# Kernel tuning notes

Measured on AMD Instinct MI355X. Metric: run time of the kernel, lower is better.

Reference implementation:

```python
import jax, jax.numpy as jnp
import numpy as np

TEMPERATURE = 0.5


def setup_inputs() -> dict:
    key = jax.random.key(0)
    k1, k2 = jax.random.split(key)
    N, D = 4096, 256
    emb_i = jax.random.normal(k1, (N, D), dtype=jnp.float32)
    emb_j = jax.random.normal(k2, (N, D), dtype=jnp.float32)
    return {"emb_i": emb_i, "emb_j": emb_j, "batch_size": N}


def reference(emb_i, emb_j, batch_size):
    N = batch_size
    # L2-normalize each embedding row (F.normalize eps=1e-12)
    def l2n(x):
        return x / jnp.maximum(jnp.linalg.norm(x, axis=1, keepdims=True), 1e-12)
    reps = jnp.concatenate([l2n(emb_i), l2n(emb_j)], axis=0)  # [2N, D]
    # cosine similarity of normalized vectors == dot product
    logits = (reps @ reps.T) / TEMPERATURE                    # [2N, 2N]
    twoN = 2 * N
    # denominator excludes only the self term k != i (stable logsumexp)
    diag_mask = jnp.eye(twoN, dtype=bool)
    masked = jnp.where(diag_mask, -jnp.inf, logits)
    log_denom = jax.nn.logsumexp(masked, axis=1)              # [2N]
    # positive pair for row i is (i+N) mod 2N
    idx = jnp.arange(twoN)
    pos = logits[idx, (idx + N) % twoN]                       # [2N]
    # loss = 1/(2N) * sum_i -log(exp(pos_i)/denom_i)
    return jnp.mean(log_denom - pos)
```

## Files before the change

kernel.cpp:

```cpp
#include <hip/hip_runtime.h>

typedef short short8 __attribute__((ext_vector_type(8)));
typedef float f32x4  __attribute__((ext_vector_type(4)));

#define TWO_N 8192
#define NHALF 4096
#define DDIM  256
#define NB    32
#define NBLK2 528

__device__ __forceinline__ float b2f(unsigned short u) {
    return __uint_as_float(((unsigned int)u) << 16);
}
__device__ __forceinline__ unsigned short f2b(float f) {
    unsigned int u = __float_as_uint(f);
    u += 0x7fffu + ((u >> 16) & 1u);
    return (unsigned short)(u >> 16);
}

__device__ __forceinline__ int probe_is_f32(const void* p, int lane) {
    unsigned int u = ((const unsigned int*)p)[lane];
    float lowv = __uint_as_float(u << 16);
    int crazy = !(fabsf(lowv) <= 1024.0f);
    return __ballot(crazy) != 0ull;
}

typedef __attribute__((address_space(1))) const unsigned int guint_t;
typedef __attribute__((address_space(3))) unsigned int luint_t;
__device__ __forceinline__ void gl_lds16(const unsigned short* g, unsigned short* l) {
    __builtin_amdgcn_global_load_lds((guint_t*)(const void*)g, (luint_t*)(void*)l, 16, 0, 0);
}

__global__ __launch_bounds__(256) void k_norm(const void* __restrict__ ei,
                                              const void* __restrict__ ej,
                                              unsigned short* __restrict__ reps) {
    int row  = (blockIdx.x * 256 + threadIdx.x) >> 6;
    int lane = threadIdx.x & 63;
    int isf  = probe_is_f32(ei, lane);
    int first = (row < NHALF);
    int r     = first ? row : row - NHALF;
    float x0, x1, x2, x3;
    if (isf) {
        const float* s = (first ? (const float*)ei : (const float*)ej) + (size_t)r * DDIM;
        float4 v = ((const float4*)s)[lane];
        x0 = v.x; x1 = v.y; x2 = v.z; x3 = v.w;
    } else {
        const unsigned short* s =
            (first ? (const unsigned short*)ei : (const unsigned short*)ej) + (size_t)r * DDIM;
        ushort4 v = ((const ushort4*)s)[lane];
        x0 = b2f(v.x); x1 = b2f(v.y); x2 = b2f(v.z); x3 = b2f(v.w);
    }
    float ss = x0 * x0 + x1 * x1 + x2 * x2 + x3 * x3;
    for (int off = 32; off > 0; off >>= 1) ss += __shfl_xor(ss, off);
    float inv = 1.0f / fmaxf(sqrtf(ss), 1e-12f);
    ushort4 o;
    o.x = f2b(x0 * inv); o.y = f2b(x1 * inv);
    o.z = f2b(x2 * inv); o.w = f2b(x3 * inv);
    ((ushort4*)(reps + (size_t)row * DDIM))[lane] = o;
}

__global__ __launch_bounds__(512, 2) void k_main(const unsigned short* __restrict__ R,
                                                 float* __restrict__ S_part,
                                                 float* __restrict__ pos) {
    __shared__ __align__(16) unsigned short As[2][256 * 64];
    __shared__ __align__(16) unsigned short Bs[2][256 * 64];

    int b = ((int)blockIdx.x & 7) * 66 + ((int)blockIdx.x >> 3);
    int rb = (int)((65.0f - sqrtf(4225.0f - 8.0f * (float)b)) * 0.5f);
    if (rb > 31) rb = 31;
    while ((65 * (rb + 1) - (rb + 1) * (rb + 1)) / 2 <= b) ++rb;
    while ((65 * rb - rb * rb) / 2 > b) --rb;
    int cb = rb + (b - (65 * rb - rb * rb) / 2);

    const int tid  = threadIdx.x;
    const int wave = tid >> 6;
    const int lane = tid & 63;
    const int quad = lane >> 4;
    const int l16  = lane & 15;
    const int wrg  = wave >> 2;
    const int wcg  = wave & 3;
    const int wr   = wrg * 128;
    const int wc   = wcg * 64;
    const int r8   = lane >> 3;
    const int c8   = (lane & 7) ^ r8;

    f32x4 acc[8][4];
#pragma unroll
    for (int r = 0; r < 8; ++r)
#pragma unroll
        for (int c = 0; c < 4; ++c) {
            acc[r][c][0] = 0.0f; acc[r][c][1] = 0.0f;
            acc[r][c][2] = 0.0f; acc[r][c][3] = 0.0f;
        }

    auto stage = [&](int d, int kc) {
#pragma unroll
        for (int t = 0; t < 4; ++t) {
            int u = wave * 4 + t;
            const unsigned short* ga =
                R + (size_t)(rb * 256 + u * 8 + r8) * DDIM + kc * 64 + c8 * 8;
            const unsigned short* gb =
                R + (size_t)(cb * 256 + u * 8 + r8) * DDIM + kc * 64 + c8 * 8;
            gl_lds16(ga, &As[d][u * 512]);
            gl_lds16(gb, &Bs[d][u * 512]);
        }
    };

    stage(0, 0);
    __syncthreads();

    for (int kc = 0; kc < 4; ++kc) {
        const int cur = kc & 1;
        if (kc < 3) stage(cur ^ 1, kc + 1);
#pragma unroll
        for (int kk = 0; kk < 2; ++kk) {
            short8 afr[8], bfr[4];
            int q  = kk * 4 + quad;
            int sl = q ^ (l16 & 7);
#pragma unroll
            for (int r = 0; r < 8; ++r)
                afr[r] = *(const short8*)(&As[cur][(wr + r * 16 + l16) * 64 + sl * 8]);
#pragma unroll
            for (int c = 0; c < 4; ++c)
                bfr[c] = *(const short8*)(&Bs[cur][(wc + c * 16 + l16) * 64 + sl * 8]);
#pragma unroll
            for (int r = 0; r < 8; ++r)
#pragma unroll
                for (int c = 0; c < 4; ++c)
                    acc[r][c] = __builtin_amdgcn_mfma_f32_16x16x32_bf16(
                        afr[r], bfr[c], acc[r][c], 0, 0, 0);
        }
        if (kc < 3) __syncthreads();
    }

    float col_acc[4][2] = {{0.0f, 0.0f}, {0.0f, 0.0f}, {0.0f, 0.0f}, {0.0f, 0.0f}};
#pragma unroll
    for (int r = 0; r < 8; ++r)
#pragma unroll
        for (int j = 0; j < 4; ++j) {
            float s = 0.0f;
#pragma unroll
            for (int c = 0; c < 4; ++c) {
                float e = __expf(fmaf(acc[r][c][j], 2.0f, -2.0f));
                s += e;
                col_acc[c][r >> 2] += e;
            }
            s += __shfl_xor(s, 1);
            s += __shfl_xor(s, 2);
            s += __shfl_xor(s, 4);
            s += __shfl_xor(s, 8);
            if (l16 == 0) {
                int row = rb * 256 + wr + r * 16 + quad * 4 + j;
                S_part[(size_t)(4 * cb + wcg) * TWO_N + row] = s;
            }
        }
    if (rb != cb) {
#pragma unroll
        for (int c = 0; c < 4; ++c)
#pragma unroll
            for (int h = 0; h < 2; ++h) {
                float s = col_acc[c][h];
                s += __shfl_xor(s, 16);
                s += __shfl_xor(s, 32);
                if (lane < 16) {
                    int row = cb * 256 + wc + c * 16 + lane;
                    S_part[(size_t)(4 * rb + 2 * wrg + h) * TWO_N + row] = s;
                }
            }
    }
    if (cb == rb + 16) {
        int dlt = (wc - wr) >> 4;
#pragma unroll
        for (int r = 0; r < 8; ++r)
#pragma unroll
            for (int c = 0; c < 4; ++c)
                if (r == c + dlt)
#pragma unroll
                    for (int j = 0; j < 4; ++j)
                        if (quad * 4 + j == l16)
                            pos[rb * 256 + wr + r * 16 + l16] = 2.0f * acc[r][c][j];
    }
}

__global__ __launch_bounds__(256) void k_rows(const float* __restrict__ S_part,
                                              const float* __restrict__ pos,
                                              float* __restrict__ part_blk) {
    __shared__ float red[256];
    int tid = threadIdx.x;
    int rr  = tid & 63;
    int cg  = tid >> 6;
    int row = blockIdx.x * 64 + rr;
    float s = 0.0f;
#pragma unroll 8
    for (int c = cg * 32; c < cg * 32 + 32; ++c)
        s += S_part[(size_t)c * TWO_N + row];
    red[tid] = s;
    __syncthreads();
    if (tid < 64) {
        float total = red[tid] + red[tid + 64] + red[tid + 128] + red[tid + 192];
        float p = (row < NHALF) ? pos[row] : pos[row - NHALF];
        float part = 2.0f + logf(total - 1.0f) - p;
        for (int off = 32; off > 0; off >>= 1) part += __shfl_xor(part, off);
        if (tid == 0) part_blk[blockIdx.x] = part;
    }
}

__global__ __launch_bounds__(128) void k_fin(const float* __restrict__ part_blk,
                                             unsigned int* __restrict__ out) {
    int tid = threadIdx.x;
    float local = part_blk[tid];
    __shared__ float red2[2];
    for (int off = 32; off > 0; off >>= 1) local += __shfl_xor(local, off);
    if ((tid & 63) == 0) red2[tid >> 6] = local;
    __syncthreads();
    if (tid == 0) {
        float L = (red2[0] + red2[1]) / 8192.0f;
        unsigned int bb = (unsigned int)f2b(L);
        out[0] = (bb << 16) | bb;
    }
}

extern "C" void kernel_launch(void* const* d_in, const int* in_sizes, int n_in,
                              void* d_out, int out_size, void* d_ws, size_t ws_size,
                              hipStream_t stream) {
    (void)in_sizes; (void)n_in; (void)out_size; (void)ws_size;
    const void* ei = d_in[0];
    const void* ej = d_in[1];
    char* ws = (char*)d_ws;

    float*          pos      = (float*)(ws);
    float*          part_blk = (float*)(ws + 16384);
    unsigned short* reps     = (unsigned short*)(ws + 49152);
    float*          S_part   = (float*)(ws + 4243456);

    k_norm<<<2048, 256, 0, stream>>>(ei, ej, reps);
    k_main<<<NBLK2, 512, 0, stream>>>(reps, S_part, pos);
    k_rows<<<128,  256, 0, stream>>>(S_part, pos, part_blk);
    k_fin <<<1,    128, 0, stream>>>(part_blk, (unsigned int*)d_out);
}
```

Baseline: 115.0 us.

## Use persistent-style grid and deeper prefetch pipeline in GEMM-exp kernel

Launches 512 blocks instead of 528, so the first 16 blocks each process two tiles, to match the grid to the CU count. The K loop now prefetches two stages ahead using raw s_barrier and explicit vmcnt waits instead of __syncthreads. It also raises wave priority around the MFMA bursts. The aim is to hide global-to-LDS latency and avoid a tail wave of 16 tiles. The trade-off is that 16 blocks do twice the work, which may lengthen the critical path.

```diff
diff --git a/kernel.cpp b/kernel.cpp
--- a/kernel.cpp
+++ b/kernel.cpp
@@ -6,8 +6,8 @@
 #define TWO_N 8192
 #define NHALF 4096
 #define DDIM  256
-#define NB    32
-#define NBLK2 528
+#define NTILE 528
+#define NBLK  512
 
 __device__ __forceinline__ float b2f(unsigned short u) {
     return __uint_as_float(((unsigned int)u) << 16);
@@ -65,13 +65,6 @@
     __shared__ __align__(16) unsigned short As[2][256 * 64];
     __shared__ __align__(16) unsigned short Bs[2][256 * 64];
 
-    int b = ((int)blockIdx.x & 7) * 66 + ((int)blockIdx.x >> 3);
-    int rb = (int)((65.0f - sqrtf(4225.0f - 8.0f * (float)b)) * 0.5f);
-    if (rb > 31) rb = 31;
-    while ((65 * (rb + 1) - (rb + 1) * (rb + 1)) / 2 <= b) ++rb;
-    while ((65 * rb - rb * rb) / 2 > b) --rb;
-    int cb = rb + (b - (65 * rb - rb * rb) / 2);
-
     const int tid  = threadIdx.x;
     const int wave = tid >> 6;
     const int lane = tid & 63;
@@ -84,101 +77,126 @@
     const int r8   = lane >> 3;
     const int c8   = (lane & 7) ^ r8;
 
-    f32x4 acc[8][4];
-#pragma unroll
-    for (int r = 0; r < 8; ++r)
-#pragma unroll
-        for (int c = 0; c < 4; ++c) {
-            acc[r][c][0] = 0.0f; acc[r][c][1] = 0.0f;
-            acc[r][c][2] = 0.0f; acc[r][c][3] = 0.0f;
+    const int bid  = (int)blockIdx.x;
+    const int nrep = (bid < NTILE - NBLK) ? 2 : 1;
+
+    for (int rep = 0; rep < nrep; ++rep) {
+        int id = (rep == 0) ? bid : bid + NBLK;
+        int b = (id & 7) * 66 + (id >> 3);
+        int rb = (int)((65.0f - sqrtf(4225.0f - 8.0f * (float)b)) * 0.5f);
+        if (rb > 31) rb = 31;
+        while ((65 * (rb + 1) - (rb + 1) * (rb + 1)) / 2 <= b) ++rb;
+        while ((65 * rb - rb * rb) / 2 > b) --rb;
+        int cb = rb + (b - (65 * rb - rb * rb) / 2);
+
+        f32x4 acc[8][4];
+#pragma unroll
+        for (int r = 0; r < 8; ++r)
+#pragma unroll
+            for (int c = 0; c < 4; ++c) {
+                acc[r][c][0] = 0.0f; acc[r][c][1] = 0.0f;
+                acc[r][c][2] = 0.0f; acc[r][c][3] = 0.0f;
+            }
+
+        auto stage = [&](int d, int kc) {
+#pragma unroll
+            for (int t = 0; t < 4; ++t) {
+                int u = wave * 4 + t;
+                const unsigned short* ga =
+                    R + (size_t)(rb * 256 + u * 8 + r8) * DDIM + kc * 64 + c8 * 8;
+                const unsigned short* gb =
+                    R + (size_t)(cb * 256 + u * 8 + r8) * DDIM + kc * 64 + c8 * 8;
+                gl_lds16(ga, &As[d][u * 512]);
+                gl_lds16(gb, &Bs[d][u * 512]);
+            }
+        };
+
+        stage(0, 0);
+        stage(1, 1);
+        asm volatile("s_waitcnt vmcnt(8)" ::: "memory");
+        __builtin_amdgcn_s_barrier();
+
+#pragma unroll
+        for (int kc = 0; kc < 4; ++kc) {
+            const int cur = kc & 1;
+#pragma unroll
+            for (int kk = 0; kk < 2; ++kk) {
+                short8 afr[8], bfr[4];
+                int q  = kk * 4 + quad;
+                int sl = q ^ (l16 & 7);
+#pragma unroll
+                for (int r = 0; r < 8; ++r)
+                    afr[r] = *(const short8*)(&As[cur][(wr + r * 16 + l16) * 64 + sl * 8]);
+#pragma unroll
+                for (int c = 0; c < 4; ++c)
+                    bfr[c] = *(const short8*)(&Bs[cur][(wc + c * 16 + l16) * 64 + sl * 8]);
+                __builtin_amdgcn_s_setprio(1);
+#pragma unroll
+                for (int r = 0; r < 8; ++r)
+#pragma unroll
+                    for (int c = 0; c < 4; ++c)
+                        acc[r][c] = __builtin_amdgcn_mfma_f32_16x16x32_bf16(
+                            afr[r], bfr[c], acc[r][c], 0, 0, 0);
+                __builtin_amdgcn_s_setprio(0);
+            }
+            __builtin_amdgcn_s_barrier();
+            if (kc + 2 < 4) stage(cur, kc + 2);
+            if (kc < 3) {
+                if (kc + 2 < 4)
+                    asm volatile("s_waitcnt vmcnt(8)" ::: "memory");
+                else
+                    asm volatile("s_waitcnt vmcnt(0)" ::: "memory");
+                __builtin_amdgcn_s_barrier();
+            }
         }
 
-    auto stage = [&](int d, int kc) {
-#pragma unroll
-        for (int t = 0; t < 4; ++t) {
-            int u = wave * 4 + t;
-            const unsigned short* ga =
-                R + (size_t)(rb * 256 + u * 8 + r8) * DDIM + kc * 64 + c8 * 8;
-            const unsigned short* gb =
-                R + (size_t)(cb * 256 + u * 8 + r8) * DDIM + kc * 64 + c8 * 8;
-            gl_lds16(ga, &As[d][u * 512]);
-            gl_lds16(gb, &Bs[d][u * 512]);
+        float col_acc[4][2] = {{0.0f, 0.0f}, {0.0f, 0.0f}, {0.0f, 0.0f}, {0.0f, 0.0f}};
+#pragma unroll
+        for (int r = 0; r < 8; ++r)
+#pragma unroll
+            for (int j = 0; j < 4; ++j) {
+                float s = 0.0f;
+#pragma unroll
+                for (int c = 0; c < 4; ++c) {
+                    float e = __expf(fmaf(acc[r][c][j], 2.0f, -2.0f));
+                    s += e;
+                    col_acc[c][r >> 2] += e;
+                }
+                s += __shfl_xor(s, 1);
+                s += __shfl_xor(s, 2);
+                s += __shfl_xor(s, 4);
+                s += __shfl_xor(s, 8);
+                if (l16 == 0) {
+                    int row = rb * 256 + wr + r * 16 + quad * 4 + j;
+                    S_part[(size_t)(4 * cb + wcg) * TWO_N + row] = s;
+                }
+            }
+        if (rb != cb) {
+#pragma unroll
+            for (int c = 0; c < 4; ++c)
+#pragma unroll
+                for (int h = 0; h < 2; ++h) {
+                    float s = col_acc[c][h];
+                    s += __shfl_xor(s, 16);
+                    s += __shfl_xor(s, 32);
+                    if (lane < 16) {
+                        int row = cb * 256 + wc + c * 16 + lane;
+                        S_part[(size_t)(4 * rb + 2 * wrg + h) * TWO_N + row] = s;
+                    }
+                }
         }
-    };
-
-    stage(0, 0);
-    __syncthreads();
-
-    for (int kc = 0; kc < 4; ++kc) {
-        const int cur = kc & 1;
-        if (kc < 3) stage(cur ^ 1, kc + 1);
-#pragma unroll
-        for (int kk = 0; kk < 2; ++kk) {
-            short8 afr[8], bfr[4];
-            int q  = kk * 4 + quad;
-            int sl = q ^ (l16 & 7);
+        if (cb == rb + 16) {
+            int dlt = (wc - wr) >> 4;
 #pragma unroll
             for (int r = 0; r < 8; ++r)
-                afr[r] = *(const short8*)(&As[cur][(wr + r * 16 + l16) * 64 + sl * 8]);
-#pragma unroll
-            for (int c = 0; c < 4; ++c)
-                bfr[c] = *(const short8*)(&Bs[cur][(wc + c * 16 + l16) * 64 + sl * 8]);
-#pragma unroll
-            for (int r = 0; r < 8; ++r)
 #pragma unroll
                 for (int c = 0; c < 4; ++c)
-                    acc[r][c] = __builtin_amdgcn_mfma_f32_16x16x32_bf16(
-                        afr[r], bfr[c], acc[r][c], 0, 0, 0);
+                    if (r == c + dlt)
+#pragma unroll
+                        for (int j = 0; j < 4; ++j)
+                            if (quad * 4 + j == l16)
+                                pos[rb * 256 + wr + r * 16 + l16] = 2.0f * acc[r][c][j];
         }
-        if (kc < 3) __syncthreads();
-    }
-
-    float col_acc[4][2] = {{0.0f, 0.0f}, {0.0f, 0.0f}, {0.0f, 0.0f}, {0.0f, 0.0f}};
-#pragma unroll
-    for (int r = 0; r < 8; ++r)
-#pragma unroll
-        for (int j = 0; j < 4; ++j) {
-            float s = 0.0f;
-#pragma unroll
-            for (int c = 0; c < 4; ++c) {
-                float e = __expf(fmaf(acc[r][c][j], 2.0f, -2.0f));
-                s += e;
-                col_acc[c][r >> 2] += e;
-            }
-            s += __shfl_xor(s, 1);
-            s += __shfl_xor(s, 2);
-            s += __shfl_xor(s, 4);
-            s += __shfl_xor(s, 8);
-            if (l16 == 0) {
-                int row = rb * 256 + wr + r * 16 + quad * 4 + j;
-                S_part[(size_t)(4 * cb + wcg) * TWO_N + row] = s;
-            }
-        }
-    if (rb != cb) {
-#pragma unroll
-        for (int c = 0; c < 4; ++c)
-#pragma unroll
-            for (int h = 0; h < 2; ++h) {
-                float s = col_acc[c][h];
-                s += __shfl_xor(s, 16);
-                s += __shfl_xor(s, 32);
-                if (lane < 16) {
-                    int row = cb * 256 + wc + c * 16 + lane;
-                    S_part[(size_t)(4 * rb + 2 * wrg + h) * TWO_N + row] = s;
-                }
-            }
-    }
-    if (cb == rb + 16) {
-        int dlt = (wc - wr) >> 4;
-#pragma unroll
-        for (int r = 0; r < 8; ++r)
-#pragma unroll
-            for (int c = 0; c < 4; ++c)
-                if (r == c + dlt)
-#pragma unroll
-                    for (int j = 0; j < 4; ++j)
-                        if (quad * 4 + j == l16)
-                            pos[rb * 256 + wr + r * 16 + l16] = 2.0f * acc[r][c][j];
     }
 }
 
@@ -234,7 +252,7 @@
     float*          S_part   = (float*)(ws + 4243456);
 
     k_norm<<<2048, 256, 0, stream>>>(ei, ej, reps);
-    k_main<<<NBLK2, 512, 0, stream>>>(reps, S_part, pos);
+    k_main<<<NBLK, 512, 0, stream>>>(reps, S_part, pos);
     k_rows<<<128,  256, 0, stream>>>(S_part, pos, part_blk);
     k_fin <<<1,    128, 0, stream>>>(part_blk, (unsigned int*)d_out);
 }
```

New measurement: 114.0 us. Within noise of the previous version (-0.9%).
